# Kernel optimization log

Hardware: AMD Instinct MI355X
Metric: run time of the kernel (lower is better)

## Reference

```python
import jax, jax.numpy as jnp
import numpy as np

B, T, D, H = 4096, 512, 1, 64

def _uniform(k, shape, scale):
    return jax.random.uniform(k, shape, jnp.float32, -scale, scale)

def setup_inputs() -> dict:
    key = jax.random.key(0)
    ks = jax.random.split(key, 12)
    s = 1.0 / np.sqrt(H)  # torch nn.LSTM init scale
    return {
        "x": jax.random.normal(ks[0], (B, T, D), jnp.float32),
        # layer 0 (input_size=D)
        "W_ih0": _uniform(ks[1], (4 * H, D), s),
        "W_hh0": _uniform(ks[2], (4 * H, H), s),
        "b_ih0": _uniform(ks[3], (4 * H,), s),
        "b_hh0": _uniform(ks[4], (4 * H,), s),
        # layer 1 (input_size=H)
        "W_ih1": _uniform(ks[5], (4 * H, H), s),
        "W_hh1": _uniform(ks[6], (4 * H, H), s),
        "b_ih1": _uniform(ks[7], (4 * H,), s),
        "b_hh1": _uniform(ks[8], (4 * H,), s),
        # final projection to scalar
        "W_fc": _uniform(ks[9], (1, H), s),
        "b_fc": _uniform(ks[10], (1,), s),
    }

def _lstm_layer(x_seq, W_ih, W_hh, b_ih, b_hh):
    # x_seq: (B, T, Din) -> hidden sequence (B, T, H). Gate order: i, f, g, o.
    b, t, _ = x_seq.shape
    h = W_hh.shape[1]
    # precompute input contribution for all timesteps: (T, B, 4H)
    x_proj = jnp.einsum('btd,gd->tbg', x_seq, W_ih) + b_ih + b_hh
    Whh_T = W_hh.T  # (H, 4H)

    def step(carry, xp):
        h_t, c_t = carry
        gates = xp + h_t @ Whh_T  # (B, 4H)
        i_g, f_g, g_g, o_g = jnp.split(gates, 4, axis=-1)
        i_g = jax.nn.sigmoid(i_g)
        f_g = jax.nn.sigmoid(f_g)
        g_g = jnp.tanh(g_g)
        o_g = jax.nn.sigmoid(o_g)
        c_t = f_g * c_t + i_g * g_g
        h_t = o_g * jnp.tanh(c_t)
        return (h_t, c_t), h_t

    h0 = jnp.zeros((b, h), x_seq.dtype)
    (_, _), hs = jax.lax.scan(step, (h0, h0), x_proj)  # hs: (T, B, H)
    return jnp.swapaxes(hs, 0, 1)

def reference(x, W_ih0, W_hh0, b_ih0, b_hh0, W_ih1, W_hh1, b_ih1, b_hh1, W_fc, b_fc):
    h1 = _lstm_layer(x, W_ih0, W_hh0, b_ih0, b_hh0)   # (B, T, H)
    h2 = _lstm_layer(h1, W_ih1, W_hh1, b_ih1, b_hh1)  # (B, T, H)
    last = h2[:, -1, :]                                # (B, H)
    return last @ W_fc.T + b_fc                        # (B, 1)
```

## Files before the change

kernel.cpp:

```cpp
#include <hip/hip_runtime.h>


#define TT 512
#define HH 64
#define NB 16
#define XP 516

typedef __bf16 bf16_t;
typedef bf16_t bf16x8 __attribute__((ext_vector_type(8)));
typedef float  f32x4  __attribute__((ext_vector_type(4)));
typedef float  f32x2  __attribute__((ext_vector_type(2)));

#define MFMA(A, B, C) __builtin_amdgcn_mfma_f32_16x16x32_bf16((A), (B), (C), 0, 0, 0)
#define RCPF(x) __builtin_amdgcn_rcpf(x)

#if __has_builtin(__builtin_amdgcn_exp2f)
#define EXP2F(x) __builtin_amdgcn_exp2f(x)
#else
__device__ __forceinline__ float EXP2F(float x) {
    float r;
    asm volatile("v_exp_f32 %0, %1" : "=v"(r) : "v"(x));
    return r;
}
#endif

#define SC_IFO (-1.4426950408889634f)
#define SC_G   ( 2.8853900817779268f)

__device__ __forceinline__ unsigned short f32_to_bf16_rne(float f) {
    unsigned int u = __builtin_bit_cast(unsigned int, f);
    unsigned int r = u + 0x7fffu + ((u >> 16) & 1u);
    return (unsigned short)(r >> 16);
}
__device__ __forceinline__ bf16_t bits_to_bf16(unsigned short u) {
    return __builtin_bit_cast(bf16_t, u);
}
__device__ __forceinline__ void build_frag_scaled(const float* __restrict__ p, float sc,
                                                  bf16x8& w) {
    const float4 a = *(const float4*)p;
    const float4 b = *(const float4*)(p + 4);
    float v[8] = {a.x, a.y, a.z, a.w, b.x, b.y, b.z, b.w};
#pragma unroll
    for (int jj = 0; jj < 8; ++jj)
        w[jj] = bits_to_bf16(f32_to_bf16_rne(v[jj] * sc));
}

__device__ __forceinline__ f32x2 exp2v(f32x2 v) {
    f32x2 r; r[0] = EXP2F(v[0]); r[1] = EXP2F(v[1]); return r;
}
__device__ __forceinline__ f32x2 rcpv(f32x2 v) {
    f32x2 r; r[0] = RCPF(v[0]); r[1] = RCPF(v[1]); return r;
}
__device__ __forceinline__ f32x2 cell2(const f32x4 a0, const f32x4 a1, f32x2* c) {
    f32x2 is = {a0[0], a1[0]}, fs = {a0[1], a1[1]};
    f32x2 gs = {a0[2], a1[2]}, os = {a0[3], a1[3]};
    const f32x2 pf = exp2v(fs);
    const f32x2 fg = rcpv(1.0f + pf);
    const f32x2 pi = exp2v(is);
    const f32x2 e2 = exp2v(gs);
    const f32x2 z  = (e2 - 1.0f) * rcpv((1.0f + pi) * (1.0f + e2));
    *c = fg * (*c) + z;
    const f32x2 po  = exp2v(os);
    const f32x2 e2c = exp2v((*c) * SC_G);
    return (e2c - 1.0f) * rcpv((1.0f + po) * (1.0f + e2c));
}

#define STEP_BARRIER()                                                          \
    do {                                                                        \
        asm volatile("s_waitcnt lgkmcnt(0)" ::: "memory");                      \
        __builtin_amdgcn_s_barrier();                                           \
        asm volatile("" ::: "memory");                                          \
    } while (0)

__global__ __launch_bounds__(1024, 4)
void lstm_1t_kernel(const float* __restrict__ x,
                    const float* __restrict__ Wih0, const float* __restrict__ Whh0,
                    const float* __restrict__ bih0, const float* __restrict__ bhh0,
                    const float* __restrict__ Wih1, const float* __restrict__ Whh1,
                    const float* __restrict__ bih1, const float* __restrict__ bhh1,
                    const float* __restrict__ Wfc,  const float* __restrict__ bfc,
                    float* __restrict__ out)
{
    __shared__ float xbuf[NB][XP];
    __shared__ unsigned short h0r[8][NB][64];
    __shared__ unsigned short h1r[2][NB][64];
    __shared__ float h1fin[HH][NB + 1];

    const int tid  = threadIdx.x;
    const int wv   = tid >> 6;
    const int lane = tid & 63;
    const int m    = lane & 15;
    const int q    = lane >> 4;
    const int m7   = m & 7;
    const int b0   = blockIdx.x * NB;
    const bool isL0 = (wv < 8);

    for (int i = tid; i < NB * TT / 4; i += 1024) {
        const int b  = i >> 7;
        const int t4 = i & 127;
        *(float4*)&xbuf[b][t4 * 4] = *(const float4*)&x[(size_t)(b0 + b) * TT + t4 * 4];
    }
    for (int i = tid; i < 8 * NB * 64; i += 1024) (&h0r[0][0][0])[i] = 0;
    for (int i = tid; i < 2 * NB * 64; i += 1024) (&h1r[0][0][0])[i] = 0;

    int roff[2];
#pragma unroll
    for (int kt = 0; kt < 2; ++kt)
        roff[kt] = m * 64 + (((4 * kt + q) ^ m7) * 8);

    const int gate_m = m & 3;
    const float scA  = (gate_m == 2) ? SC_G : SC_IFO;
    unsigned short* const H0 = &h0r[0][0][0];
    unsigned short* const H1 = &h1r[0][0][0];

    __syncthreads();

    if (isL0) {
        const int w = wv;
        bf16x8 Ah[2][2];
        f32x4 bb0s[2], wx0s[2];
        int woff[2];
#pragma unroll
        for (int tau = 0; tau < 2; ++tau) {
            const int rowA = 64 * gate_m + 8 * w + 4 * tau + (m >> 2);
#pragma unroll
            for (int kt = 0; kt < 2; ++kt)
                build_frag_scaled(&Whh0[rowA * HH + kt * 32 + q * 8], scA, Ah[tau][kt]);
#pragma unroll
            for (int r = 0; r < 4; ++r) {
                const int row = 64 * r + 8 * w + 4 * tau + q;
                const float sc = (r == 2) ? SC_G : SC_IFO;
                bb0s[tau][r] = (bih0[row] + bhh0[row]) * sc;
                wx0s[tau][r] = Wih0[row] * sc;
            }
            const int u = 8 * w + 4 * tau + q;
            woff[tau] = m * 64 + (((u >> 3) ^ m7) * 8) + (u & 7);
        }

        f32x2 cA = {0.f, 0.f};

#pragma unroll 1
        for (int tt = 0; tt <= TT; ++tt) {
            if (tt < TT) {
                const int rs = ((tt - 1) & 7) * (NB * 64);
                bf16x8 h0[2];
                h0[0] = *(const bf16x8*)(H0 + rs + roff[0]);
                h0[1] = *(const bf16x8*)(H0 + rs + roff[1]);

                const float xv = xbuf[m][tt];
                f32x4 a[2];
#pragma unroll
                for (int tau = 0; tau < 2; ++tau) {
#pragma unroll
                    for (int r = 0; r < 4; ++r)
                        a[tau][r] = __builtin_fmaf(xv, wx0s[tau][r], bb0s[tau][r]);
                }

#pragma unroll
                for (int tau = 0; tau < 2; ++tau) {
                    f32x4 z = {0.f, 0.f, 0.f, 0.f};
                    a[tau] = MFMA(Ah[tau][0], h0[0], a[tau]);
                    z      = MFMA(Ah[tau][1], h0[1], z);
                    a[tau] = a[tau] + z;
                }

                const f32x2 hv = cell2(a[0], a[1], &cA);

                const int ws = (tt & 7) * (NB * 64);
                H0[ws + woff[0]] = f32_to_bf16_rne(hv[0]);
                H0[ws + woff[1]] = f32_to_bf16_rne(hv[1]);
            }
            STEP_BARRIER();
        }
    } else {
        const int uW = wv - 8;
        bf16x8 Ah[2][4];
        f32x4 bb1s[2];
        int woff[2], uu[2];
#pragma unroll
        for (int tau = 0; tau < 2; ++tau) {
            const int rowA = 64 * gate_m + 8 * uW + 4 * tau + (m >> 2);
#pragma unroll
            for (int kt = 0; kt < 2; ++kt)
                build_frag_scaled(&Wih1[rowA * HH + kt * 32 + q * 8], scA, Ah[tau][kt]);
#pragma unroll
            for (int kt = 0; kt < 2; ++kt)
                build_frag_scaled(&Whh1[rowA * HH + kt * 32 + q * 8], scA, Ah[tau][2 + kt]);
#pragma unroll
            for (int r = 0; r < 4; ++r) {
                const int row = 64 * r + 8 * uW + 4 * tau + q;
                const float sc = (r == 2) ? SC_G : SC_IFO;
                bb1s[tau][r] = (bih1[row] + bhh1[row]) * sc;
            }
            const int u = 8 * uW + 4 * tau + q;
            uu[tau]   = u;
            woff[tau] = m * 64 + (((u >> 3) ^ m7) * 8) + (u & 7);
        }

        f32x2 c1v = {0.f, 0.f};

#pragma unroll 1
        for (int tt = 0; tt <= TT; ++tt) {
            if (tt >= 1) {
                const int tm = tt - 1;
                const int rs0 = (tm & 7) * (NB * 64);
                const int rs1 = ((tm - 1) & 1) * (NB * 64);
                bf16x8 h0[2], h1[2];
                h0[0] = *(const bf16x8*)(H0 + rs0 + roff[0]);
                h0[1] = *(const bf16x8*)(H0 + rs0 + roff[1]);
                h1[0] = *(const bf16x8*)(H1 + rs1 + roff[0]);
                h1[1] = *(const bf16x8*)(H1 + rs1 + roff[1]);

                f32x4 a[2];
#pragma unroll
                for (int tau = 0; tau < 2; ++tau) {
                    a[tau] = MFMA(Ah[tau][0], h0[0], bb1s[tau]);
                    a[tau] = MFMA(Ah[tau][1], h0[1], a[tau]);
                    a[tau] = MFMA(Ah[tau][2], h1[0], a[tau]);
                    a[tau] = MFMA(Ah[tau][3], h1[1], a[tau]);
                }

                const f32x2 hv = cell2(a[0], a[1], &c1v);
                if (tm == TT - 1) {
                    h1fin[uu[0]][m] = hv[0];
                    h1fin[uu[1]][m] = hv[1];
                }
                const int ws = (tm & 1) * (NB * 64);
                H1[ws + woff[0]] = f32_to_bf16_rne(hv[0]);
                H1[ws + woff[1]] = f32_to_bf16_rne(hv[1]);
            }
            STEP_BARRIER();
        }
    }

    __syncthreads();

    if (tid < NB) {
        float sacc = bfc[0];
#pragma unroll
        for (int u = 0; u < HH; ++u) sacc = fmaf(h1fin[u][tid], Wfc[u], sacc);
        out[b0 + tid] = sacc;
    }
}

extern "C" void kernel_launch(void* const* d_in, const int* in_sizes, int n_in,
                              void* d_out, int out_size, void* d_ws, size_t ws_size,
                              hipStream_t stream) {
    const float* x    = (const float*)d_in[0];
    const float* Wih0 = (const float*)d_in[1];
    const float* Whh0 = (const float*)d_in[2];
    const float* bih0 = (const float*)d_in[3];
    const float* bhh0 = (const float*)d_in[4];
    const float* Wih1 = (const float*)d_in[5];
    const float* Whh1 = (const float*)d_in[6];
    const float* bih1 = (const float*)d_in[7];
    const float* bhh1 = (const float*)d_in[8];
    const float* Wfc  = (const float*)d_in[9];
    const float* bfc  = (const float*)d_in[10];

    lstm_1t_kernel<<<dim3(4096 / NB), dim3(1024), 0, stream>>>(
        x, Wih0, Whh0, bih0, bhh0, Wih1, Whh1, bih1, bhh1, Wfc, bfc, (float*)d_out);
}
```

Baseline: 420.1 us.

## Merge layer-0 and layer-1 waves so each wave computes both LSTM layers

The block shrinks from 1024 to 512 threads, and each of the 8 waves now computes both layer 0 at step t and layer 1 at step t-1 inside one loop, instead of using separate wave groups for each layer. This halves the number of waves taking part in each per-step barrier and lets one wave interleave the MFMAs and transcendental work of the two layers, which is meant to cut barrier and synchronisation cost. In exchange, each wave holds both layers' weight fragments in registers and does more serial work per step, and the per-step critical path may lengthen.

```diff
diff --git a/kernel.cpp b/kernel.cpp
--- a/kernel.cpp
+++ b/kernel.cpp
@@ -72,7 +72,7 @@
         asm volatile("" ::: "memory");                                          \
     } while (0)
 
-__global__ __launch_bounds__(1024, 4)
+__global__ __launch_bounds__(512, 2)
 void lstm_1t_kernel(const float* __restrict__ x,
                     const float* __restrict__ Wih0, const float* __restrict__ Whh0,
                     const float* __restrict__ bih0, const float* __restrict__ bhh0,
@@ -93,15 +93,14 @@
     const int q    = lane >> 4;
     const int m7   = m & 7;
     const int b0   = blockIdx.x * NB;
-    const bool isL0 = (wv < 8);
-
-    for (int i = tid; i < NB * TT / 4; i += 1024) {
+
+    for (int i = tid; i < NB * TT / 4; i += 512) {
         const int b  = i >> 7;
         const int t4 = i & 127;
         *(float4*)&xbuf[b][t4 * 4] = *(const float4*)&x[(size_t)(b0 + b) * TT + t4 * 4];
     }
-    for (int i = tid; i < 8 * NB * 64; i += 1024) (&h0r[0][0][0])[i] = 0;
-    for (int i = tid; i < 2 * NB * 64; i += 1024) (&h1r[0][0][0])[i] = 0;
+    for (int i = tid; i < 8 * NB * 64; i += 512) (&h0r[0][0][0])[i] = 0;
+    for (int i = tid; i < 2 * NB * 64; i += 512) (&h1r[0][0][0])[i] = 0;
 
     int roff[2];
 #pragma unroll
@@ -113,124 +112,103 @@
     unsigned short* const H0 = &h0r[0][0][0];
     unsigned short* const H1 = &h1r[0][0][0];
 
+    const int w = wv;
+    bf16x8 Ah0[2][2];
+    f32x4 bb0s[2], wx0s[2];
+    int woff0[2];
+#pragma unroll
+    for (int tau = 0; tau < 2; ++tau) {
+        const int rowA = 64 * gate_m + 8 * w + 4 * tau + (m >> 2);
+#pragma unroll
+        for (int kt = 0; kt < 2; ++kt)
+            build_frag_scaled(&Whh0[rowA * HH + kt * 32 + q * 8], scA, Ah0[tau][kt]);
+#pragma unroll
+        for (int r = 0; r < 4; ++r) {
+            const int row = 64 * r + 8 * w + 4 * tau + q;
+            const float sc = (r == 2) ? SC_G : SC_IFO;
+            bb0s[tau][r] = (bih0[row] + bhh0[row]) * sc;
+            wx0s[tau][r] = Wih0[row] * sc;
+        }
+        const int u = 8 * w + 4 * tau + q;
+        woff0[tau] = m * 64 + (((u >> 3) ^ m7) * 8) + (u & 7);
+    }
+
+    bf16x8 Ah1[2][4];
+    f32x4 bb1s[2];
+    int woff1[2], uu[2];
+#pragma unroll
+    for (int tau = 0; tau < 2; ++tau) {
+        const int rowA = 64 * gate_m + 8 * w + 4 * tau + (m >> 2);
+#pragma unroll
+        for (int kt = 0; kt < 2; ++kt)
+            build_frag_scaled(&Wih1[rowA * HH + kt * 32 + q * 8], scA, Ah1[tau][kt]);
+#pragma unroll
+        for (int kt = 0; kt < 2; ++kt)
+            build_frag_scaled(&Whh1[rowA * HH + kt * 32 + q * 8], scA, Ah1[tau][2 + kt]);
+#pragma unroll
+        for (int r = 0; r < 4; ++r) {
+            const int row = 64 * r + 8 * w + 4 * tau + q;
+            const float sc = (r == 2) ? SC_G : SC_IFO;
+            bb1s[tau][r] = (bih1[row] + bhh1[row]) * sc;
+        }
+        const int u = 8 * w + 4 * tau + q;
+        uu[tau]   = u;
+        woff1[tau] = m * 64 + (((u >> 3) ^ m7) * 8) + (u & 7);
+    }
+
+    f32x2 cA  = {0.f, 0.f};
+    f32x2 c1v = {0.f, 0.f};
+
     __syncthreads();
 
-    if (isL0) {
-        const int w = wv;
-        bf16x8 Ah[2][2];
-        f32x4 bb0s[2], wx0s[2];
-        int woff[2];
-#pragma unroll
-        for (int tau = 0; tau < 2; ++tau) {
-            const int rowA = 64 * gate_m + 8 * w + 4 * tau + (m >> 2);
-#pragma unroll
-            for (int kt = 0; kt < 2; ++kt)
-                build_frag_scaled(&Whh0[rowA * HH + kt * 32 + q * 8], scA, Ah[tau][kt]);
-#pragma unroll
-            for (int r = 0; r < 4; ++r) {
-                const int row = 64 * r + 8 * w + 4 * tau + q;
-                const float sc = (r == 2) ? SC_G : SC_IFO;
-                bb0s[tau][r] = (bih0[row] + bhh0[row]) * sc;
-                wx0s[tau][r] = Wih0[row] * sc;
+#pragma unroll 1
+    for (int tt = 0; tt <= TT; ++tt) {
+        const int rs0 = ((tt - 1) & 7) * (NB * 64);
+        const int rs1 = ((tt - 2) & 1) * (NB * 64);
+        bf16x8 h0[2], h1[2];
+        h0[0] = *(const bf16x8*)(H0 + rs0 + roff[0]);
+        h0[1] = *(const bf16x8*)(H0 + rs0 + roff[1]);
+        h1[0] = *(const bf16x8*)(H1 + rs1 + roff[0]);
+        h1[1] = *(const bf16x8*)(H1 + rs1 + roff[1]);
+
+        if (tt < TT) {
+            const float xv = xbuf[m][tt];
+            f32x4 a0[2];
+#pragma unroll
+            for (int tau = 0; tau < 2; ++tau) {
+#pragma unroll
+                for (int r = 0; r < 4; ++r)
+                    a0[tau][r] = __builtin_fmaf(xv, wx0s[tau][r], bb0s[tau][r]);
+                a0[tau] = MFMA(Ah0[tau][0], h0[0], a0[tau]);
+                a0[tau] = MFMA(Ah0[tau][1], h0[1], a0[tau]);
             }
-            const int u = 8 * w + 4 * tau + q;
-            woff[tau] = m * 64 + (((u >> 3) ^ m7) * 8) + (u & 7);
-        }
-
-        f32x2 cA = {0.f, 0.f};
-
-#pragma unroll 1
-        for (int tt = 0; tt <= TT; ++tt) {
-            if (tt < TT) {
-                const int rs = ((tt - 1) & 7) * (NB * 64);
-                bf16x8 h0[2];
-                h0[0] = *(const bf16x8*)(H0 + rs + roff[0]);
-                h0[1] = *(const bf16x8*)(H0 + rs + roff[1]);
-
-                const float xv = xbuf[m][tt];
-                f32x4 a[2];
-#pragma unroll
-                for (int tau = 0; tau < 2; ++tau) {
-#pragma unroll
-                    for (int r = 0; r < 4; ++r)
-                        a[tau][r] = __builtin_fmaf(xv, wx0s[tau][r], bb0s[tau][r]);
-                }
-
-#pragma unroll
-                for (int tau = 0; tau < 2; ++tau) {
-                    f32x4 z = {0.f, 0.f, 0.f, 0.f};
-                    a[tau] = MFMA(Ah[tau][0], h0[0], a[tau]);
-                    z      = MFMA(Ah[tau][1], h0[1], z);
-                    a[tau] = a[tau] + z;
-                }
-
-                const f32x2 hv = cell2(a[0], a[1], &cA);
-
-                const int ws = (tt & 7) * (NB * 64);
-                H0[ws + woff[0]] = f32_to_bf16_rne(hv[0]);
-                H0[ws + woff[1]] = f32_to_bf16_rne(hv[1]);
+            const f32x2 hv0 = cell2(a0[0], a0[1], &cA);
+            const int ws = (tt & 7) * (NB * 64);
+            H0[ws + woff0[0]] = f32_to_bf16_rne(hv0[0]);
+            H0[ws + woff0[1]] = f32_to_bf16_rne(hv0[1]);
+        }
+
+        if (tt >= 1) {
+            const int tm = tt - 1;
+            f32x4 a1[2];
+#pragma unroll
+            for (int tau = 0; tau < 2; ++tau) {
+                a1[tau] = MFMA(Ah1[tau][0], h0[0], bb1s[tau]);
+                a1[tau] = MFMA(Ah1[tau][1], h0[1], a1[tau]);
+                a1[tau] = MFMA(Ah1[tau][2], h1[0], a1[tau]);
+                a1[tau] = MFMA(Ah1[tau][3], h1[1], a1[tau]);
             }
-            STEP_BARRIER();
-        }
-    } else {
-        const int uW = wv - 8;
-        bf16x8 Ah[2][4];
-        f32x4 bb1s[2];
-        int woff[2], uu[2];
-#pragma unroll
-        for (int tau = 0; tau < 2; ++tau) {
-            const int rowA = 64 * gate_m + 8 * uW + 4 * tau + (m >> 2);
-#pragma unroll
-            for (int kt = 0; kt < 2; ++kt)
-                build_frag_scaled(&Wih1[rowA * HH + kt * 32 + q * 8], scA, Ah[tau][kt]);
-#pragma unroll
-            for (int kt = 0; kt < 2; ++kt)
-                build_frag_scaled(&Whh1[rowA * HH + kt * 32 + q * 8], scA, Ah[tau][2 + kt]);
-#pragma unroll
-            for (int r = 0; r < 4; ++r) {
-                const int row = 64 * r + 8 * uW + 4 * tau + q;
-                const float sc = (r == 2) ? SC_G : SC_IFO;
-                bb1s[tau][r] = (bih1[row] + bhh1[row]) * sc;
+            const f32x2 hv1 = cell2(a1[0], a1[1], &c1v);
+            if (tm == TT - 1) {
+                h1fin[uu[0]][m] = hv1[0];
+                h1fin[uu[1]][m] = hv1[1];
             }
-            const int u = 8 * uW + 4 * tau + q;
-            uu[tau]   = u;
-            woff[tau] = m * 64 + (((u >> 3) ^ m7) * 8) + (u & 7);
-        }
-
-        f32x2 c1v = {0.f, 0.f};
-
-#pragma unroll 1
-        for (int tt = 0; tt <= TT; ++tt) {
-            if (tt >= 1) {
-                const int tm = tt - 1;
-                const int rs0 = (tm & 7) * (NB * 64);
-                const int rs1 = ((tm - 1) & 1) * (NB * 64);
-                bf16x8 h0[2], h1[2];
-                h0[0] = *(const bf16x8*)(H0 + rs0 + roff[0]);
-                h0[1] = *(const bf16x8*)(H0 + rs0 + roff[1]);
-                h1[0] = *(const bf16x8*)(H1 + rs1 + roff[0]);
-                h1[1] = *(const bf16x8*)(H1 + rs1 + roff[1]);
-
-                f32x4 a[2];
-#pragma unroll
-                for (int tau = 0; tau < 2; ++tau) {
-                    a[tau] = MFMA(Ah[tau][0], h0[0], bb1s[tau]);
-                    a[tau] = MFMA(Ah[tau][1], h0[1], a[tau]);
-                    a[tau] = MFMA(Ah[tau][2], h1[0], a[tau]);
-                    a[tau] = MFMA(Ah[tau][3], h1[1], a[tau]);
-                }
-
-                const f32x2 hv = cell2(a[0], a[1], &c1v);
-                if (tm == TT - 1) {
-                    h1fin[uu[0]][m] = hv[0];
-                    h1fin[uu[1]][m] = hv[1];
-                }
-                const int ws = (tm & 1) * (NB * 64);
-                H1[ws + woff[0]] = f32_to_bf16_rne(hv[0]);
-                H1[ws + woff[1]] = f32_to_bf16_rne(hv[1]);
-            }
-            STEP_BARRIER();
-        }
+            const int ws = (tm & 1) * (NB * 64);
+            H1[ws + woff1[0]] = f32_to_bf16_rne(hv1[0]);
+            H1[ws + woff1[1]] = f32_to_bf16_rne(hv1[1]);
+        }
+
+        STEP_BARRIER();
     }
 
     __syncthreads();
@@ -258,6 +236,6 @@
     const float* Wfc  = (const float*)d_in[9];
     const float* bfc  = (const float*)d_in[10];
 
-    lstm_1t_kernel<<<dim3(4096 / NB), dim3(1024), 0, stream>>>(
+    lstm_1t_kernel<<<dim3(4096 / NB), dim3(512), 0, stream>>>(
         x, Wih0, Whh0, bih0, bhh0, Wih1, Whh1, bih1, bhh1, Wfc, bfc, (float*)d_out);
 }
```

Measured after the change: 465.8 us. 1.11x slower.

## Shrink LSTM block to 4 waves with per-gate MFMA tiles and bias folded into MFMA

Applied to the files above, without the earlier changes.

Work is repartitioned from 16 waves (8 per layer) to 4 waves (2 per layer) per block. Each wave now computes 16-row tiles per gate with weights held in registers. The input projection and bias are folded into an extra MFMA using hi/lo bf16 splits, and hidden-state stores are packed into 64-bit LDS writes. The h0 ring buffer shrinks from 8 slots to 2. The aim is cheaper barriers and less per-step overhead, at the cost of more MFMAs per wave, higher register pressure, and a longer serial chain per step.

```diff
diff --git a/kernel.cpp b/kernel.cpp
--- a/kernel.cpp
+++ b/kernel.cpp
@@ -34,6 +34,10 @@
 }
 __device__ __forceinline__ bf16_t bits_to_bf16(unsigned short u) {
     return __builtin_bit_cast(bf16_t, u);
+}
+__device__ __forceinline__ float bf16_bits_to_f32(unsigned short u) {
+    unsigned int v = ((unsigned int)u) << 16;
+    return __builtin_bit_cast(float, v);
 }
 __device__ __forceinline__ void build_frag_scaled(const float* __restrict__ p, float sc,
                                                   bf16x8& w) {
@@ -72,7 +76,7 @@
         asm volatile("" ::: "memory");                                          \
     } while (0)
 
-__global__ __launch_bounds__(1024, 4)
+__global__ __launch_bounds__(256, 1)
 void lstm_1t_kernel(const float* __restrict__ x,
                     const float* __restrict__ Wih0, const float* __restrict__ Whh0,
                     const float* __restrict__ bih0, const float* __restrict__ bhh0,
@@ -82,152 +86,202 @@
                     float* __restrict__ out)
 {
     __shared__ float xbuf[NB][XP];
-    __shared__ unsigned short h0r[8][NB][64];
-    __shared__ unsigned short h1r[2][NB][64];
+    __shared__ unsigned short h0s[2][NB][64];
+    __shared__ unsigned short h1s[2][NB][64];
     __shared__ float h1fin[HH][NB + 1];
 
     const int tid  = threadIdx.x;
     const int wv   = tid >> 6;
     const int lane = tid & 63;
-    const int m    = lane & 15;
+    const int c    = lane & 15;
     const int q    = lane >> 4;
-    const int m7   = m & 7;
+    const int c7   = c & 7;
     const int b0   = blockIdx.x * NB;
-    const bool isL0 = (wv < 8);
-
-    for (int i = tid; i < NB * TT / 4; i += 1024) {
+    const bool isL0 = (wv < 2);
+    const int jbase = (wv & 1) * 2;
+
+    for (int i = tid; i < NB * TT / 4; i += 256) {
         const int b  = i >> 7;
         const int t4 = i & 127;
         *(float4*)&xbuf[b][t4 * 4] = *(const float4*)&x[(size_t)(b0 + b) * TT + t4 * 4];
     }
-    for (int i = tid; i < 8 * NB * 64; i += 1024) (&h0r[0][0][0])[i] = 0;
-    for (int i = tid; i < 2 * NB * 64; i += 1024) (&h1r[0][0][0])[i] = 0;
+    for (int i = tid; i < 2 * NB * 64; i += 256) {
+        (&h0s[0][0][0])[i] = 0;
+        (&h1s[0][0][0])[i] = 0;
+    }
 
     int roff[2];
 #pragma unroll
     for (int kt = 0; kt < 2; ++kt)
-        roff[kt] = m * 64 + (((4 * kt + q) ^ m7) * 8);
-
-    const int gate_m = m & 3;
-    const float scA  = (gate_m == 2) ? SC_G : SC_IFO;
-    unsigned short* const H0 = &h0r[0][0][0];
-    unsigned short* const H1 = &h1r[0][0][0];
+        roff[kt] = c * 64 + (((4 * kt + q) ^ c7) * 8);
+    int woff[2];
+#pragma unroll
+    for (int jj = 0; jj < 2; ++jj) {
+        const int j = jbase + jj;
+        woff[jj] = c * 64 + (((2 * j + (q >> 1)) ^ c7) * 8) + 4 * (q & 1);
+    }
+
+    unsigned short* const H0 = &h0s[0][0][0];
+    unsigned short* const H1 = &h1s[0][0][0];
 
     __syncthreads();
 
     if (isL0) {
-        const int w = wv;
-        bf16x8 Ah[2][2];
-        f32x4 bb0s[2], wx0s[2];
-        int woff[2];
-#pragma unroll
-        for (int tau = 0; tau < 2; ++tau) {
-            const int rowA = 64 * gate_m + 8 * w + 4 * tau + (m >> 2);
-#pragma unroll
-            for (int kt = 0; kt < 2; ++kt)
-                build_frag_scaled(&Whh0[rowA * HH + kt * 32 + q * 8], scA, Ah[tau][kt]);
-#pragma unroll
-            for (int r = 0; r < 4; ++r) {
-                const int row = 64 * r + 8 * w + 4 * tau + q;
-                const float sc = (r == 2) ? SC_G : SC_IFO;
-                bb0s[tau][r] = (bih0[row] + bhh0[row]) * sc;
-                wx0s[tau][r] = Wih0[row] * sc;
+        bf16x8 Wf[2][4][2];
+        bf16x8 F3[2][4];
+#pragma unroll
+        for (int jj = 0; jj < 2; ++jj) {
+            const int j = jbase + jj;
+#pragma unroll
+            for (int g = 0; g < 4; ++g) {
+                const int row = 64 * g + 16 * j + c;
+                const float sc = (g == 2) ? SC_G : SC_IFO;
+#pragma unroll
+                for (int kt = 0; kt < 2; ++kt)
+                    build_frag_scaled(&Whh0[row * HH + kt * 32 + q * 8], sc, Wf[jj][g][kt]);
+                const float wxs = Wih0[row] * sc;
+                const float bbs = (bih0[row] + bhh0[row]) * sc;
+                const unsigned short wxh = f32_to_bf16_rne(wxs);
+                const unsigned short wxl = f32_to_bf16_rne(wxs - bf16_bits_to_f32(wxh));
+                const unsigned short bh  = f32_to_bf16_rne(bbs);
+                const unsigned short bl  = f32_to_bf16_rne(bbs - bf16_bits_to_f32(bh));
+                bf16x8 f;
+#pragma unroll
+                for (int e = 0; e < 8; ++e) f[e] = bits_to_bf16(0);
+                if (q == 0) {
+                    f[0] = bits_to_bf16(wxh); f[1] = bits_to_bf16(wxh);
+                    f[2] = bits_to_bf16(wxl);
+                    f[3] = bits_to_bf16(bh);  f[4] = bits_to_bf16(bl);
+                }
+                F3[jj][g] = f;
             }
-            const int u = 8 * w + 4 * tau + q;
-            woff[tau] = m * 64 + (((u >> 3) ^ m7) * 8) + (u & 7);
         }
 
-        f32x2 cA = {0.f, 0.f};
+        f32x2 cst[4] = {{0.f, 0.f}, {0.f, 0.f}, {0.f, 0.f}, {0.f, 0.f}};
 
 #pragma unroll 1
         for (int tt = 0; tt <= TT; ++tt) {
             if (tt < TT) {
-                const int rs = ((tt - 1) & 7) * (NB * 64);
-                bf16x8 h0[2];
-                h0[0] = *(const bf16x8*)(H0 + rs + roff[0]);
-                h0[1] = *(const bf16x8*)(H0 + rs + roff[1]);
-
-                const float xv = xbuf[m][tt];
-                f32x4 a[2];
-#pragma unroll
-                for (int tau = 0; tau < 2; ++tau) {
-#pragma unroll
-                    for (int r = 0; r < 4; ++r)
-                        a[tau][r] = __builtin_fmaf(xv, wx0s[tau][r], bb0s[tau][r]);
-                }
-
-#pragma unroll
-                for (int tau = 0; tau < 2; ++tau) {
-                    f32x4 z = {0.f, 0.f, 0.f, 0.f};
-                    a[tau] = MFMA(Ah[tau][0], h0[0], a[tau]);
-                    z      = MFMA(Ah[tau][1], h0[1], z);
-                    a[tau] = a[tau] + z;
-                }
-
-                const f32x2 hv = cell2(a[0], a[1], &cA);
-
-                const int ws = (tt & 7) * (NB * 64);
-                H0[ws + woff[0]] = f32_to_bf16_rne(hv[0]);
-                H0[ws + woff[1]] = f32_to_bf16_rne(hv[1]);
+                const int rs = ((tt - 1) & 1) * (NB * 64);
+                const bf16x8 h0f0 = *(const bf16x8*)(H0 + rs + roff[0]);
+                const bf16x8 h0f1 = *(const bf16x8*)(H0 + rs + roff[1]);
+
+                const float xv = xbuf[c][tt];
+                const unsigned short xh = f32_to_bf16_rne(xv);
+                const unsigned short xl = f32_to_bf16_rne(xv - bf16_bits_to_f32(xh));
+                bf16x8 b3;
+#pragma unroll
+                for (int e = 0; e < 8; ++e) b3[e] = bits_to_bf16(0);
+                if (q == 0) {
+                    b3[0] = bits_to_bf16(xh); b3[1] = bits_to_bf16(xl);
+                    b3[2] = bits_to_bf16(xh);
+                    b3[3] = bits_to_bf16(0x3F80); b3[4] = bits_to_bf16(0x3F80);
+                }
+
+                const int ws = (tt & 1) * (NB * 64);
+#pragma unroll
+                for (int jj = 0; jj < 2; ++jj) {
+                    f32x4 acc[4];
+#pragma unroll
+                    for (int g = 0; g < 4; ++g) {
+                        f32x4 z = {0.f, 0.f, 0.f, 0.f};
+                        z = MFMA(F3[jj][g], b3, z);
+                        z = MFMA(Wf[jj][g][1], h0f1, z);
+                        acc[g] = MFMA(Wf[jj][g][0], h0f0, z);
+                    }
+                    const f32x4 g0 = {acc[0][0], acc[1][0], acc[2][0], acc[3][0]};
+                    const f32x4 g1 = {acc[0][1], acc[1][1], acc[2][1], acc[3][1]};
+                    const f32x4 g2 = {acc[0][2], acc[1][2], acc[2][2], acc[3][2]};
+                    const f32x4 g3 = {acc[0][3], acc[1][3], acc[2][3], acc[3][3]};
+                    const f32x2 hvA = cell2(g0, g1, &cst[jj * 2]);
+                    const f32x2 hvB = cell2(g2, g3, &cst[jj * 2 + 1]);
+                    const unsigned int lo = (unsigned int)f32_to_bf16_rne(hvA[0]) |
+                                            ((unsigned int)f32_to_bf16_rne(hvA[1]) << 16);
+                    const unsigned int hi = (unsigned int)f32_to_bf16_rne(hvB[0]) |
+                                            ((unsigned int)f32_to_bf16_rne(hvB[1]) << 16);
+                    uint2 v; v.x = lo; v.y = hi;
+                    *(uint2*)(H0 + ws + woff[jj]) = v;
+                }
             }
             STEP_BARRIER();
         }
     } else {
-        const int uW = wv - 8;
-        bf16x8 Ah[2][4];
-        f32x4 bb1s[2];
-        int woff[2], uu[2];
-#pragma unroll
-        for (int tau = 0; tau < 2; ++tau) {
-            const int rowA = 64 * gate_m + 8 * uW + 4 * tau + (m >> 2);
-#pragma unroll
-            for (int kt = 0; kt < 2; ++kt)
-                build_frag_scaled(&Wih1[rowA * HH + kt * 32 + q * 8], scA, Ah[tau][kt]);
-#pragma unroll
-            for (int kt = 0; kt < 2; ++kt)
-                build_frag_scaled(&Whh1[rowA * HH + kt * 32 + q * 8], scA, Ah[tau][2 + kt]);
-#pragma unroll
-            for (int r = 0; r < 4; ++r) {
-                const int row = 64 * r + 8 * uW + 4 * tau + q;
-                const float sc = (r == 2) ? SC_G : SC_IFO;
-                bb1s[tau][r] = (bih1[row] + bhh1[row]) * sc;
+        bf16x8 Wi[2][4][2];
+        bf16x8 Wh[2][4][2];
+        bf16x8 BA[2][4];
+#pragma unroll
+        for (int jj = 0; jj < 2; ++jj) {
+            const int j = jbase + jj;
+#pragma unroll
+            for (int g = 0; g < 4; ++g) {
+                const int row = 64 * g + 16 * j + c;
+                const float sc = (g == 2) ? SC_G : SC_IFO;
+#pragma unroll
+                for (int kt = 0; kt < 2; ++kt) {
+                    build_frag_scaled(&Wih1[row * HH + kt * 32 + q * 8], sc, Wi[jj][g][kt]);
+                    build_frag_scaled(&Whh1[row * HH + kt * 32 + q * 8], sc, Wh[jj][g][kt]);
+                }
+                const float bbs = (bih1[row] + bhh1[row]) * sc;
+                const unsigned short bh = f32_to_bf16_rne(bbs);
+                const unsigned short bl = f32_to_bf16_rne(bbs - bf16_bits_to_f32(bh));
+                bf16x8 f;
+#pragma unroll
+                for (int e = 0; e < 8; ++e) f[e] = bits_to_bf16(0);
+                if (q == 0) { f[0] = bits_to_bf16(bh); f[1] = bits_to_bf16(bl); }
+                BA[jj][g] = f;
             }
-            const int u = 8 * uW + 4 * tau + q;
-            uu[tau]   = u;
-            woff[tau] = m * 64 + (((u >> 3) ^ m7) * 8) + (u & 7);
         }
-
-        f32x2 c1v = {0.f, 0.f};
+        bf16x8 Bone;
+#pragma unroll
+        for (int e = 0; e < 8; ++e) Bone[e] = bits_to_bf16(0);
+        if (q == 0) { Bone[0] = bits_to_bf16(0x3F80); Bone[1] = bits_to_bf16(0x3F80); }
+
+        f32x2 cst[4] = {{0.f, 0.f}, {0.f, 0.f}, {0.f, 0.f}, {0.f, 0.f}};
 
 #pragma unroll 1
         for (int tt = 0; tt <= TT; ++tt) {
             if (tt >= 1) {
                 const int tm = tt - 1;
-                const int rs0 = (tm & 7) * (NB * 64);
+                const int rs0 = (tm & 1) * (NB * 64);
                 const int rs1 = ((tm - 1) & 1) * (NB * 64);
-                bf16x8 h0[2], h1[2];
-                h0[0] = *(const bf16x8*)(H0 + rs0 + roff[0]);
-                h0[1] = *(const bf16x8*)(H0 + rs0 + roff[1]);
-                h1[0] = *(const bf16x8*)(H1 + rs1 + roff[0]);
-                h1[1] = *(const bf16x8*)(H1 + rs1 + roff[1]);
-
-                f32x4 a[2];
-#pragma unroll
-                for (int tau = 0; tau < 2; ++tau) {
-                    a[tau] = MFMA(Ah[tau][0], h0[0], bb1s[tau]);
-                    a[tau] = MFMA(Ah[tau][1], h0[1], a[tau]);
-                    a[tau] = MFMA(Ah[tau][2], h1[0], a[tau]);
-                    a[tau] = MFMA(Ah[tau][3], h1[1], a[tau]);
-                }
-
-                const f32x2 hv = cell2(a[0], a[1], &c1v);
-                if (tm == TT - 1) {
-                    h1fin[uu[0]][m] = hv[0];
-                    h1fin[uu[1]][m] = hv[1];
-                }
+                const bf16x8 h0f0 = *(const bf16x8*)(H0 + rs0 + roff[0]);
+                const bf16x8 h0f1 = *(const bf16x8*)(H0 + rs0 + roff[1]);
+                const bf16x8 h1f0 = *(const bf16x8*)(H1 + rs1 + roff[0]);
+                const bf16x8 h1f1 = *(const bf16x8*)(H1 + rs1 + roff[1]);
+
                 const int ws = (tm & 1) * (NB * 64);
-                H1[ws + woff[0]] = f32_to_bf16_rne(hv[0]);
-                H1[ws + woff[1]] = f32_to_bf16_rne(hv[1]);
+#pragma unroll
+                for (int jj = 0; jj < 2; ++jj) {
+                    f32x4 acc[4];
+#pragma unroll
+                    for (int g = 0; g < 4; ++g) {
+                        f32x4 z = {0.f, 0.f, 0.f, 0.f};
+                        z = MFMA(BA[jj][g], Bone, z);
+                        z = MFMA(Wh[jj][g][1], h1f1, z);
+                        z = MFMA(Wh[jj][g][0], h1f0, z);
+                        z = MFMA(Wi[jj][g][1], h0f1, z);
+                        acc[g] = MFMA(Wi[jj][g][0], h0f0, z);
+                    }
+                    const f32x4 g0 = {acc[0][0], acc[1][0], acc[2][0], acc[3][0]};
+                    const f32x4 g1 = {acc[0][1], acc[1][1], acc[2][1], acc[3][1]};
+                    const f32x4 g2 = {acc[0][2], acc[1][2], acc[2][2], acc[3][2]};
+                    const f32x4 g3 = {acc[0][3], acc[1][3], acc[2][3], acc[3][3]};
+                    const f32x2 hvA = cell2(g0, g1, &cst[jj * 2]);
+                    const f32x2 hvB = cell2(g2, g3, &cst[jj * 2 + 1]);
+                    if (tm == TT - 1) {
+                        const int ub = 16 * (jbase + jj) + 4 * q;
+                        h1fin[ub + 0][c] = hvA[0];
+                        h1fin[ub + 1][c] = hvA[1];
+                        h1fin[ub + 2][c] = hvB[0];
+                        h1fin[ub + 3][c] = hvB[1];
+                    }
+                    const unsigned int lo = (unsigned int)f32_to_bf16_rne(hvA[0]) |
+                                            ((unsigned int)f32_to_bf16_rne(hvA[1]) << 16);
+                    const unsigned int hi = (unsigned int)f32_to_bf16_rne(hvB[0]) |
+                                            ((unsigned int)f32_to_bf16_rne(hvB[1]) << 16);
+                    uint2 v; v.x = lo; v.y = hi;
+                    *(uint2*)(H1 + ws + woff[jj]) = v;
+                }
             }
             STEP_BARRIER();
         }
@@ -258,6 +312,6 @@
     const float* Wfc  = (const float*)d_in[9];
     const float* bfc  = (const float*)d_in[10];
 
-    lstm_1t_kernel<<<dim3(4096 / NB), dim3(1024), 0, stream>>>(
+    lstm_1t_kernel<<<dim3(4096 / NB), dim3(256), 0, stream>>>(
         x, Wih0, Whh0, bih0, bhh0, Wih1, Whh1, bih1, bhh1, Wfc, bfc, (float*)d_out);
 }
```

Result: slower. 500.3 us (+19.1%).
